# Kernel optimization log

Hardware: AMD Instinct MI355X
Metric: run time of the kernel (lower is better)

The kernel has to match this reference:

```python
import jax, jax.numpy as jnp
import numpy as np
import math

B, N, E, H, DEPTH, MLP_RATIO, A = 8, 1024, 768, 12, 6, 4, 7
F = MLP_RATIO * E


def _get_attention_slopes(n):
    def p2(n):
        start = 2 ** (-2 ** (-(math.log2(n) - 3)))
        return [start * start ** i for i in range(n)]
    if math.log2(n).is_integer():
        return p2(n)
    c = 2 ** math.floor(math.log2(n))
    return p2(c) + _get_attention_slopes(2 * c)[0::2][: n - c]


def _ln(x, scale, bias, eps=1e-6):
    m = jnp.mean(x, axis=-1, keepdims=True)
    v = jnp.var(x, axis=-1, keepdims=True)
    return (x - m) * jax.lax.rsqrt(v + eps) * scale + bias


def setup_inputs() -> dict:
    key = jax.random.key(0)
    ks = jax.random.split(key, 8)
    s = 0.02
    return {
        "x": jax.random.normal(ks[0], (B, N, E), jnp.float32),
        "ln1_scale": jnp.ones((DEPTH, E), jnp.float32),
        "ln1_bias": jnp.zeros((DEPTH, E), jnp.float32),
        "wqkv": jax.random.normal(ks[1], (DEPTH, E, 3 * E), jnp.float32) * s,
        "bqkv": jnp.zeros((DEPTH, 3 * E), jnp.float32),
        "wo": jax.random.normal(ks[2], (DEPTH, E, E), jnp.float32) * s,
        "bo": jnp.zeros((DEPTH, E), jnp.float32),
        "ln2_scale": jnp.ones((DEPTH, E), jnp.float32),
        "ln2_bias": jnp.zeros((DEPTH, E), jnp.float32),
        "w1": jax.random.normal(ks[3], (DEPTH, E, F), jnp.float32) * s,
        "w2": jax.random.normal(ks[4], (DEPTH, F, E), jnp.float32) * s,
        "lnf_scale": jnp.ones((E,), jnp.float32),
        "lnf_bias": jnp.zeros((E,), jnp.float32),
        "head_w1": jax.random.normal(ks[5], (E, E), jnp.float32) * s,
        "head_b1": jnp.zeros((E,), jnp.float32),
        "head_w2": jax.random.normal(ks[6], (E, A), jnp.float32) * s,
    }


def reference(x, ln1_scale, ln1_bias, wqkv, bqkv, wo, bo, ln2_scale, ln2_bias, w1, w2, lnf_scale, lnf_bias, head_w1, head_b1, head_w2):
    b, n, e = x.shape
    h = H
    dh = e // h
    scale = dh ** (-0.5)
    # ALiBi bias: slopes[h] * key-position (exactly as original code computes it)
    slopes = jnp.asarray(_get_attention_slopes(h), x.dtype)
    pos_bias = slopes[None, :, None, None] * jnp.arange(n, dtype=x.dtype)[None, None, None, :]
    causal = jnp.tril(jnp.ones((n, n), bool))[None, None]  # [1,1,n,n]
    big_neg = jnp.finfo(x.dtype).min

    depth = ln1_scale.shape[0]
    for i in range(depth):
        y = _ln(x, ln1_scale[i], ln1_bias[i])
        qkv = y @ wqkv[i] + bqkv[i]
        q, k, v = jnp.split(qkv, 3, axis=-1)
        q = q.reshape(b, n, h, dh).transpose(0, 2, 1, 3)  # b h n d
        k = k.reshape(b, n, h, dh).transpose(0, 2, 1, 3)
        v = v.reshape(b, n, h, dh).transpose(0, 2, 1, 3)
        att = jnp.einsum('bhnd,bhmd->bhnm', q, k) * scale + pos_bias
        att = jnp.where(causal, att, big_neg)
        att = jax.nn.softmax(att, axis=-1)
        o = jnp.einsum('bhnm,bhmd->bhnd', att, v)
        o = o.transpose(0, 2, 1, 3).reshape(b, n, e)
        x = x + (o @ wo[i] + bo[i])
        y = _ln(x, ln2_scale[i], ln2_bias[i])
        y = jax.nn.gelu(y @ w1[i])  # flax default: tanh-approx gelu; FF has no bias
        x = x + y @ w2[i]
    x = _ln(x, lnf_scale, lnf_bias)
    actions = jax.nn.relu(x @ head_w1 + head_b1) @ head_w2
    return actions
```

## Files before the change

kernel.cpp:

```cpp
#include <hip/hip_runtime.h>
#include <hip/hip_bf16.h>
#include <cstdint>

#define DEV __device__ __forceinline__

typedef __bf16 bf16x8 __attribute__((ext_vector_type(8)));
typedef float f32x4 __attribute__((ext_vector_type(4)));
typedef unsigned short u16;
typedef u16 u16x8 __attribute__((ext_vector_type(8)));
typedef u16 u16x4 __attribute__((ext_vector_type(4)));
typedef uint32_t u32x2 __attribute__((ext_vector_type(2)));

DEV u16 f2bf(float f) {
  union { float f; uint32_t u; } a; a.f = f;
  uint32_t u = a.u + 0x7fffu + ((a.u >> 16) & 1u);
  return (u16)(u >> 16);
}
DEV float b2f(u16 v) {
  union { uint32_t u; float f; } a; a.u = ((uint32_t)v) << 16;
  return a.f;
}

DEV float fexp2(float x) {
#if __has_builtin(__builtin_amdgcn_exp2f)
  return __builtin_amdgcn_exp2f(x);
#else
  return __expf(x * 0.69314718056f);
#endif
}

DEV uint32_t cvtpk(float lo, float hi) {
  uint32_t r;
  asm("v_cvt_pk_bf16_f32 %0, %1, %2" : "=v"(r) : "v"(lo), "v"(hi));
  return r;
}

DEV void gload16(const void* g, void* lds) {
  __builtin_amdgcn_global_load_lds((__attribute__((address_space(1))) void*)g,
                                   (__attribute__((address_space(3))) void*)lds,
                                   16, 0, 0);
}

DEV void nts8(u16* p, u16x8 v) {
  __builtin_nontemporal_store(v, (u16x8*)p);
}

struct TMat { const float* src; u16* dst; int K; int N; int t0; };
struct TArgs { TMat m[26]; int nmat; };

__global__ __launch_bounds__(256) void transpose_all(TArgs args) {
  __shared__ float tile[64][65];
  const int bid = blockIdx.x;
  int i = 0;
  #pragma unroll 1
  for (int t = 1; t < args.nmat; ++t) if (bid >= args.m[t].t0) i = t;
  const TMat mm = args.m[i];
  const int tid = bid - mm.t0;
  const int ntx = mm.N >> 6;
  const int tx = tid % ntx, ty = tid / ntx;
  const int n0 = tx * 64, k0 = ty * 64;
  const int c = threadIdx.x & 63, r0 = threadIdx.x >> 6;
  #pragma unroll
  for (int s = 0; s < 16; ++s) {
    int r = r0 + s * 4;
    tile[r][c] = mm.src[(size_t)(k0 + r) * mm.N + n0 + c];
  }
  __syncthreads();
  #pragma unroll
  for (int s = 0; s < 16; ++s) {
    int rr = r0 + s * 4;
    mm.dst[(size_t)(n0 + rr) * mm.K + k0 + c] = f2bf(tile[c][rr]);
  }
}

__global__ __launch_bounds__(256) void ln_kernel(const float* __restrict__ x,
                                                 const float* __restrict__ sc,
                                                 const float* __restrict__ bi,
                                                 u16* __restrict__ y, int Mtok) {
  const int bid = blockIdx.x;
  const int tok = ((bid & 7) << 10) + ((bid >> 3) << 2) + (threadIdx.x >> 6);
  const int l = threadIdx.x & 63;
  if (tok >= Mtok) return;
  const float4* row = (const float4*)(x + (size_t)tok * 768);
  float4 a = row[l], b = row[l + 64], cc = row[l + 128];
  float s = a.x + a.y + a.z + a.w + b.x + b.y + b.z + b.w + cc.x + cc.y + cc.z + cc.w;
  float q = a.x*a.x + a.y*a.y + a.z*a.z + a.w*a.w
          + b.x*b.x + b.y*b.y + b.z*b.z + b.w*b.w
          + cc.x*cc.x + cc.y*cc.y + cc.z*cc.z + cc.w*cc.w;
  #pragma unroll
  for (int off = 1; off < 64; off <<= 1) { s += __shfl_xor(s, off); q += __shfl_xor(q, off); }
  const float mean = s * (1.f / 768.f);
  const float var = q * (1.f / 768.f) - mean * mean;
  const float r = rsqrtf(var + 1e-6f);
  u16* yr = y + (size_t)tok * 768;
  #pragma unroll
  for (int p = 0; p < 3; ++p) {
    const int col0 = 4 * (l + 64 * p);
    float4 v = (p == 0) ? a : (p == 1) ? b : cc;
    float4 scv = *(const float4*)(sc + col0);
    float4 biv = *(const float4*)(bi + col0);
    u16x4 o;
    o[0] = f2bf((v.x - mean) * r * scv.x + biv.x);
    o[1] = f2bf((v.y - mean) * r * scv.y + biv.y);
    o[2] = f2bf((v.z - mean) * r * scv.z + biv.z);
    o[3] = f2bf((v.w - mean) * r * scv.w + biv.w);
    *(u16x4*)(yr + col0) = o;
  }
}

enum { EPI_BF16 = 0, EPI_RESID = 1, EPI_GELU = 2, EPI_RELU = 3 };

__global__ __launch_bounds__(256, 2) void gemm128(
    const u16* __restrict__ A, const u16* __restrict__ Bt,
    const float* __restrict__ bias, const float* __restrict__ resid,
    float* __restrict__ outF, u16* __restrict__ outB,
    int N, int K, int nxb, int epi) {
  __shared__ u16 smem[32768];
  const int tid = threadIdx.x;
  const int w = tid >> 6, l = tid & 63;

  const int nwg = gridDim.x;
  const int flat = blockIdx.x;
  const int wg = (flat & 7) * (nwg >> 3) + (flat >> 3);
  const int bx = wg % nxb, by = wg / nxb;
  const int m0 = by << 7, n0 = bx << 7;

  const int wr = (w >> 1) << 6, wc = (w & 1) << 6;
  const int cl = l & 15, g = l >> 4;
  f32x4 acc[4][4] = {};

  const int lrow = l >> 3;
  const int scol = ((l & 7) ^ lrow) << 3;
  const u16* agp = A  + (size_t)(m0 + (w << 5) + lrow) * K + scol;
  const u16* bgp = Bt + (size_t)(n0 + (w << 5) + lrow) * K + scol;
  const int ldso = w << 11;
  const int nkt = K >> 6;

  #pragma unroll
  for (int q = 0; q < 4; ++q) {
    gload16(agp + (size_t)(q * 8) * K, &smem[ldso + (q << 9)]);
    gload16(bgp + (size_t)(q * 8) * K, &smem[16384 + ldso + (q << 9)]);
  }

  const int sw = cl & 7;
  for (int kt = 0; kt < nkt; ++kt) {
    const int cur = kt & 1;
    if (kt + 1 < nkt) {
      const size_t koff = (size_t)(kt + 1) << 6;
      const int nb = (cur ^ 1) << 13;
      #pragma unroll
      for (int q = 0; q < 4; ++q) {
        gload16(agp + koff + (size_t)(q * 8) * K, &smem[nb + ldso + (q << 9)]);
        gload16(bgp + koff + (size_t)(q * 8) * K, &smem[16384 + nb + ldso + (q << 9)]);
      }
      asm volatile("s_waitcnt vmcnt(8)" ::: "memory");
    } else {
      asm volatile("s_waitcnt vmcnt(0)" ::: "memory");
    }
    __builtin_amdgcn_s_barrier();
    __builtin_amdgcn_sched_barrier(0);
    const u16* Ab = &smem[cur << 13];
    const u16* Bb = &smem[16384 + (cur << 13)];
    #pragma unroll
    for (int ks = 0; ks < 2; ++ks) {
      bf16x8 af[4], bfr[4];
      const int ps = (((ks << 2) | g) ^ sw) << 3;
      #pragma unroll
      for (int mt = 0; mt < 4; ++mt)
        af[mt] = *(const bf16x8*)(Ab + ((wr + mt * 16 + cl) << 6) + ps);
      #pragma unroll
      for (int nt = 0; nt < 4; ++nt)
        bfr[nt] = *(const bf16x8*)(Bb + ((wc + nt * 16 + cl) << 6) + ps);
      #pragma unroll
      for (int mt = 0; mt < 4; ++mt)
        #pragma unroll
        for (int nt = 0; nt < 4; ++nt)
          acc[mt][nt] = __builtin_amdgcn_mfma_f32_16x16x32_bf16(af[mt], bfr[nt], acc[mt][nt], 0, 0, 0);
    }
    asm volatile("s_waitcnt lgkmcnt(0)" ::: "memory");
    __builtin_amdgcn_s_barrier();
  }

  float* scr = (float*)smem + w * 1056;
  const int rg = g << 2;
  const int er = l >> 3;
  const int ec0 = (l & 7) << 3;
  #pragma unroll
  for (int mt = 0; mt < 4; ++mt) {
    #pragma unroll
    for (int nt = 0; nt < 4; ++nt)
      #pragma unroll
      for (int j = 0; j < 4; ++j)
        scr[(rg + j) * 66 + nt * 16 + cl] = acc[mt][nt][j];
    #pragma unroll
    for (int t = 0; t < 2; ++t) {
      const int r = (t << 3) + er;
      const int grow = m0 + wr + mt * 16 + r;
      const int gcol = n0 + wc + ec0;
      float v[8];
      #pragma unroll
      for (int u = 0; u < 8; ++u) v[u] = scr[r * 66 + ec0 + u];
      if (bias) {
        #pragma unroll
        for (int u = 0; u < 8; ++u) v[u] += bias[gcol + u];
      }
      if (epi == EPI_RESID) {
        const float* rp = resid + (size_t)grow * N + gcol;
        float* op = outF + (size_t)grow * N + gcol;
        float4 o0, o1;
        o0.x = v[0] + rp[0]; o0.y = v[1] + rp[1]; o0.z = v[2] + rp[2]; o0.w = v[3] + rp[3];
        o1.x = v[4] + rp[4]; o1.y = v[5] + rp[5]; o1.z = v[6] + rp[6]; o1.w = v[7] + rp[7];
        *(float4*)op = o0;
        *(float4*)(op + 4) = o1;
      } else {
        u16x8 ov;
        #pragma unroll
        for (int u = 0; u < 8; ++u) {
          float x = v[u];
          if (epi == EPI_GELU) {
            const float e = __expf(-(1.5957691216f * x + 0.0713548163f * x * x * x));
            x = x / (1.f + e);
          } else if (epi == EPI_RELU) {
            x = fmaxf(x, 0.f);
          }
          ov[u] = f2bf(x);
        }
        if (epi == EPI_BF16 || epi == EPI_GELU)
          nts8(outB + (size_t)grow * N + gcol, ov);
        else
          *(u16x8*)(outB + (size_t)grow * N + gcol) = ov;
      }
    }
  }
}

__global__ __launch_bounds__(512, 2) void attn_kernel(const u16* __restrict__ qkv,
                                                      u16* __restrict__ o) {
  __shared__ u16 Ksm[2][4096];
  __shared__ u16 Vt[2][64][68];
  __shared__ u16 P[8][16][72];
  const int flat = blockIdx.x;
  const int b = flat & 7;
  const int rr = flat >> 3;
  const int h = rr >> 3;
  const int j = rr & 7;
  const int tid = threadIdx.x;
  const int w = tid >> 6, l = tid & 63;
  const int cl = l & 15, lg = l >> 4;
  const int qtile = (w < 4) ? j : 15 - j;
  const int q0 = qtile * 64 + (w & 3) * 16;
  const int rowg = q0 + cl;
  const float log2e = 1.44269504f;
  const float scale2 = 0.125f * log2e;
  const float slope = (h < 8) ? exp2f(-(float)(h + 1)) : exp2f(-0.5f - (float)(h - 8));
  const float slope2 = slope * log2e;
  const size_t rs_ = 2304;
  const size_t bbase = (size_t)b * 1024 * rs_;

  const u16* qp = qkv + bbase + (size_t)rowg * rs_ + h * 64 + lg * 8;
  bf16x8 qa0 = *(const bf16x8*)qp;
  bf16x8 qa1 = *(const bf16x8*)(qp + 32);

  float m_r = -1e30f, l_r = 0.f;
  f32x4 oacc[4];
  #pragma unroll
  for (int d = 0; d < 4; ++d) oacc[d] = (f32x4){0.f, 0.f, 0.f, 0.f};

  const u16* ksrc = qkv + bbase + (size_t)(tid >> 3) * rs_ + 768 + h * 64 +
                    (((tid & 7) ^ ((tid >> 3) & 7)) << 3);
  const int vd0 = w << 3;
  const u16* vbase = qkv + bbase + (size_t)l * rs_ + 1536 + h * 64 + vd0;

  const int nkv = 16 - j;
  gload16(ksrc, &Ksm[0][w << 9]);
  u16x8 vreg = *(const u16x8*)vbase;
  __syncthreads();

  const int sw = cl & 7;
  const int ps0 = (lg ^ sw) << 3;
  const int ps1 = ps0 ^ 32;

  for (int kv = 0; kv < nkv; ++kv) {
    const int buf = kv & 1;
    #pragma unroll
    for (int i = 0; i < 8; ++i) Vt[buf][vd0 + i][l] = vreg[i];
    u16x8 vnext = vreg;
    if (kv + 1 < nkv) {
      gload16(ksrc + (size_t)(kv + 1) * 64 * rs_, &Ksm[buf ^ 1][w << 9]);
      vnext = *(const u16x8*)(vbase + (size_t)(kv + 1) * 64 * rs_);
    }

    const bool active = (kv <= qtile);
    bf16x8 pa0, pa1;
    if (active) {
      const u16* Kb = &Ksm[buf][0];
      f32x4 pp[4];
      float pm = -3.0e38f;
      __builtin_amdgcn_s_setprio(1);
      #pragma unroll
      for (int nt = 0; nt < 4; ++nt) {
        const int row = nt * 16 + cl;
        bf16x8 bk0 = *(const bf16x8*)(Kb + (row << 6) + ps0);
        bf16x8 bk1 = *(const bf16x8*)(Kb + (row << 6) + ps1);
        f32x4 s = (f32x4){0.f, 0.f, 0.f, 0.f};
        s = __builtin_amdgcn_mfma_f32_16x16x32_bf16(bk0, qa0, s, 0, 0, 0);
        s = __builtin_amdgcn_mfma_f32_16x16x32_bf16(bk1, qa1, s, 0, 0, 0);
        const int kb = kv * 64 + nt * 16 + (lg << 2);
        #pragma unroll
        for (int jj = 0; jj < 4; ++jj) {
          const int colg = kb + jj;
          float v = s[jj] * scale2 + slope2 * (float)colg;
          pp[nt][jj] = (colg <= rowg) ? v : -3.0e38f;
        }
        pm = fmaxf(pm, fmaxf(fmaxf(pp[nt][0], pp[nt][1]),
                             fmaxf(pp[nt][2], pp[nt][3])));
      }
      __builtin_amdgcn_s_setprio(0);
      pm = fmaxf(pm, __shfl_xor(pm, 16));
      pm = fmaxf(pm, __shfl_xor(pm, 32));
      const float mnew = fmaxf(m_r, pm);
      const float al = fexp2(m_r - mnew);
      m_r = mnew;
      float rs = 0.f;
      #pragma unroll
      for (int nt = 0; nt < 4; ++nt) {
        #pragma unroll
        for (int jj = 0; jj < 4; ++jj) {
          float p = fexp2(pp[nt][jj] - m_r);
          pp[nt][jj] = p;
          rs += p;
        }
      }
      rs += __shfl_xor(rs, 16);
      rs += __shfl_xor(rs, 32);
      l_r = l_r * al + rs;
      float a4[4];
      #pragma unroll
      for (int jj = 0; jj < 4; ++jj) a4[jj] = __shfl(al, (lg << 2) + jj);
      #pragma unroll
      for (int d = 0; d < 4; ++d)
        #pragma unroll
        for (int jj = 0; jj < 4; ++jj) oacc[d][jj] *= a4[jj];
      #pragma unroll
      for (int nt = 0; nt < 4; ++nt) {
        u32x2 pr;
        pr[0] = cvtpk(pp[nt][0], pp[nt][1]);
        pr[1] = cvtpk(pp[nt][2], pp[nt][3]);
        *(u32x2*)&P[w][cl][nt * 16 + (lg << 2)] = pr;
      }
      pa0 = *(const bf16x8*)&P[w][cl][lg * 8];
      pa1 = *(const bf16x8*)&P[w][cl][32 + lg * 8];
    }

    __syncthreads();

    if (active) {
      __builtin_amdgcn_s_setprio(1);
      #pragma unroll
      for (int d = 0; d < 4; ++d) {
        bf16x8 bv0 = *(const bf16x8*)&Vt[buf][d * 16 + cl][lg * 8];
        bf16x8 bv1 = *(const bf16x8*)&Vt[buf][d * 16 + cl][32 + lg * 8];
        oacc[d] = __builtin_amdgcn_mfma_f32_16x16x32_bf16(pa0, bv0, oacc[d], 0, 0, 0);
        oacc[d] = __builtin_amdgcn_mfma_f32_16x16x32_bf16(pa1, bv1, oacc[d], 0, 0, 0);
      }
      __builtin_amdgcn_s_setprio(0);
    }
    vreg = vnext;
  }

  const float linv = 1.f / l_r;
  float i4[4];
  #pragma unroll
  for (int jj = 0; jj < 4; ++jj) i4[jj] = __shfl(linv, (lg << 2) + jj);
  u16* op = o + ((size_t)b * 1024 + q0) * 768 + h * 64;
  #pragma unroll
  for (int d = 0; d < 4; ++d)
    #pragma unroll
    for (int jj = 0; jj < 4; ++jj)
      op[(size_t)((lg << 2) + jj) * 768 + d * 16 + cl] = f2bf(oacc[d][jj] * i4[jj]);
}

__global__ __launch_bounds__(256) void head2_kernel(const u16* __restrict__ act,
                                                    const float* __restrict__ w,
                                                    float* __restrict__ out, int Mtok) {
  const int bid = blockIdx.x;
  const int tok = ((bid & 7) << 10) + ((bid >> 3) << 2) + (threadIdx.x >> 6);
  const int l = threadIdx.x & 63;
  if (tok >= Mtok) return;
  float s[7] = {0.f, 0.f, 0.f, 0.f, 0.f, 0.f, 0.f};
  const u16* ar = act + (size_t)tok * 768;
  #pragma unroll
  for (int i = 0; i < 12; ++i) {
    const int k = l + i * 64;
    const float a = b2f(ar[k]);
    #pragma unroll
    for (int j = 0; j < 7; ++j) s[j] += a * w[k * 7 + j];
  }
  #pragma unroll
  for (int off = 32; off; off >>= 1)
    #pragma unroll
    for (int j = 0; j < 7; ++j) s[j] += __shfl_down(s[j], off);
  if (l == 0) {
    #pragma unroll
    for (int j = 0; j < 7; ++j) out[(size_t)tok * 7 + j] = s[j];
  }
}

extern "C" void kernel_launch(void* const* d_in, const int* in_sizes, int n_in,
                              void* d_out, int out_size, void* d_ws, size_t ws_size,
                              hipStream_t stream) {
  const float* x_in = (const float*)d_in[0];
  const float* ln1s = (const float*)d_in[1];
  const float* ln1b = (const float*)d_in[2];
  const float* wqkv = (const float*)d_in[3];
  const float* bqkv = (const float*)d_in[4];
  const float* wo   = (const float*)d_in[5];
  const float* bo   = (const float*)d_in[6];
  const float* ln2s = (const float*)d_in[7];
  const float* ln2b = (const float*)d_in[8];
  const float* w1   = (const float*)d_in[9];
  const float* w2   = (const float*)d_in[10];
  const float* lnfs = (const float*)d_in[11];
  const float* lnfb = (const float*)d_in[12];
  const float* hw1  = (const float*)d_in[13];
  const float* hb1  = (const float*)d_in[14];
  const float* hw2  = (const float*)d_in[15];
  float* out = (float*)d_out;

  const int Mtok = 8192, E = 768, E3 = 2304, F = 3072, DEPTH = 6;

  char* ws = (char*)d_ws;
  size_t off = 0;
  auto alloc = [&](size_t bytes) -> char* {
    char* p = ws + off; off += (bytes + 255) & ~(size_t)255; return p;
  };
  u16*  wqkvt = (u16*)alloc((size_t)DEPTH * E3 * E * 2);
  u16*  wot   = (u16*)alloc((size_t)DEPTH * E * E * 2);
  u16*  w1t   = (u16*)alloc((size_t)DEPTH * F * E * 2);
  u16*  w2t   = (u16*)alloc((size_t)DEPTH * E * F * 2);
  u16*  hw1t  = (u16*)alloc((size_t)E * E * 2);
  float* xb   = (float*)alloc((size_t)Mtok * E * 4);
  u16*  yb    = (u16*)alloc((size_t)Mtok * E * 2);
  u16*  big   = (u16*)alloc((size_t)Mtok * F * 2);
  (void)ws_size; (void)in_sizes; (void)n_in; (void)out_size;

  TArgs ta; int nm = 0; int t0 = 0;
  auto add = [&](const float* s, u16* d, int K, int N) {
    ta.m[nm].src = s; ta.m[nm].dst = d; ta.m[nm].K = K; ta.m[nm].N = N; ta.m[nm].t0 = t0;
    t0 += (N / 64) * (K / 64); ++nm;
  };
  for (int i = 0; i < DEPTH; ++i) add(wqkv + (size_t)i * E * E3, wqkvt + (size_t)i * E3 * E, E, E3);
  for (int i = 0; i < DEPTH; ++i) add(wo + (size_t)i * E * E, wot + (size_t)i * E * E, E, E);
  for (int i = 0; i < DEPTH; ++i) add(w1 + (size_t)i * E * F, w1t + (size_t)i * F * E, E, F);
  for (int i = 0; i < DEPTH; ++i) add(w2 + (size_t)i * F * E, w2t + (size_t)i * E * F, F, E);
  add(hw1, hw1t, E, E);
  ta.nmat = nm;
  transpose_all<<<t0, 256, 0, stream>>>(ta);

  u16* qkvb = big;
  for (int i = 0; i < DEPTH; ++i) {
    const float* xsrc = (i == 0) ? x_in : xb;
    ln_kernel<<<Mtok / 4, 256, 0, stream>>>(xsrc, ln1s + i * E, ln1b + i * E, yb, Mtok);
    gemm128<<<18 * 64, 256, 0, stream>>>(yb, wqkvt + (size_t)i * E3 * E, bqkv + (size_t)i * E3,
                                         nullptr, nullptr, qkvb, E3, E, 18, EPI_BF16);
    attn_kernel<<<768, 512, 0, stream>>>(qkvb, yb);
    gemm128<<<6 * 64, 256, 0, stream>>>(yb, wot + (size_t)i * E * E, bo + (size_t)i * E,
                                        xsrc, xb, nullptr, E, E, 6, EPI_RESID);
    ln_kernel<<<Mtok / 4, 256, 0, stream>>>(xb, ln2s + i * E, ln2b + i * E, yb, Mtok);
    gemm128<<<24 * 64, 256, 0, stream>>>(yb, w1t + (size_t)i * F * E, nullptr,
                                         nullptr, nullptr, big, F, E, 24, EPI_GELU);
    gemm128<<<6 * 64, 256, 0, stream>>>(big, w2t + (size_t)i * E * F, nullptr,
                                        xb, xb, nullptr, E, F, 6, EPI_RESID);
  }
  ln_kernel<<<Mtok / 4, 256, 0, stream>>>(xb, lnfs, lnfb, yb, Mtok);
  gemm128<<<6 * 64, 256, 0, stream>>>(yb, hw1t, hb1, nullptr, nullptr, big,
                                      E, E, 6, EPI_RELU);
  head2_kernel<<<Mtok / 4, 256, 0, stream>>>(big, hw2, out, Mtok);
}
```

Measured before the change: 1.477 ms.

## Store residual stream in bf16 and skip unneeded softmax rescales

The residual stream buffer changes from fp32 to bf16. The input is converted once, LayerNorm reads bf16, and the residual GEMM epilogues read and write bf16, which halves residual memory traffic. The bf16 packing now uses the hardware cvt_pk instruction. In attention, the running-max rescale of the accumulators is skipped when no new row max exceeds the old one by a threshold, saving exp and multiply work. Accumulating the residual in bf16 over 12 layers loses precision and could hurt accuracy.

```diff
diff --git a/kernel.cpp b/kernel.cpp
--- a/kernel.cpp
+++ b/kernel.cpp
@@ -10,6 +10,7 @@
 typedef u16 u16x8 __attribute__((ext_vector_type(8)));
 typedef u16 u16x4 __attribute__((ext_vector_type(4)));
 typedef uint32_t u32x2 __attribute__((ext_vector_type(2)));
+typedef uint32_t u32x4 __attribute__((ext_vector_type(4)));
 
 DEV u16 f2bf(float f) {
   union { float f; uint32_t u; } a; a.f = f;
@@ -39,10 +40,6 @@
   __builtin_amdgcn_global_load_lds((__attribute__((address_space(1))) void*)g,
                                    (__attribute__((address_space(3))) void*)lds,
                                    16, 0, 0);
-}
-
-DEV void nts8(u16* p, u16x8 v) {
-  __builtin_nontemporal_store(v, (u16x8*)p);
 }
 
 struct TMat { const float* src; u16* dst; int K; int N; int t0; };
@@ -73,7 +70,18 @@
   }
 }
 
-__global__ __launch_bounds__(256) void ln_kernel(const float* __restrict__ x,
+__global__ __launch_bounds__(256) void f2b_kernel(const float4* __restrict__ in,
+                                                  u32x4* __restrict__ out, int n8) {
+  const int i = blockIdx.x * 256 + threadIdx.x;
+  if (i >= n8) return;
+  float4 a = in[2 * i], b = in[2 * i + 1];
+  u32x4 o;
+  o[0] = cvtpk(a.x, a.y); o[1] = cvtpk(a.z, a.w);
+  o[2] = cvtpk(b.x, b.y); o[3] = cvtpk(b.z, b.w);
+  out[i] = o;
+}
+
+__global__ __launch_bounds__(256) void ln_kernel(const u16* __restrict__ x,
                                                  const float* __restrict__ sc,
                                                  const float* __restrict__ bi,
                                                  u16* __restrict__ y, int Mtok) {
@@ -81,40 +89,50 @@
   const int tok = ((bid & 7) << 10) + ((bid >> 3) << 2) + (threadIdx.x >> 6);
   const int l = threadIdx.x & 63;
   if (tok >= Mtok) return;
-  const float4* row = (const float4*)(x + (size_t)tok * 768);
-  float4 a = row[l], b = row[l + 64], cc = row[l + 128];
-  float s = a.x + a.y + a.z + a.w + b.x + b.y + b.z + b.w + cc.x + cc.y + cc.z + cc.w;
-  float q = a.x*a.x + a.y*a.y + a.z*a.z + a.w*a.w
-          + b.x*b.x + b.y*b.y + b.z*b.z + b.w*b.w
-          + cc.x*cc.x + cc.y*cc.y + cc.z*cc.z + cc.w*cc.w;
+  const u16* row = x + (size_t)tok * 768;
+  u16x8 v0 = *(const u16x8*)(row + l * 8);
+  u16x4 v1 = *(const u16x4*)(row + 512 + l * 4);
+  float f[12];
+  #pragma unroll
+  for (int i = 0; i < 8; ++i) f[i] = b2f(v0[i]);
+  #pragma unroll
+  for (int i = 0; i < 4; ++i) f[8 + i] = b2f(v1[i]);
+  float s = 0.f, q = 0.f;
+  #pragma unroll
+  for (int i = 0; i < 12; ++i) { s += f[i]; q += f[i] * f[i]; }
   #pragma unroll
   for (int off = 1; off < 64; off <<= 1) { s += __shfl_xor(s, off); q += __shfl_xor(q, off); }
   const float mean = s * (1.f / 768.f);
   const float var = q * (1.f / 768.f) - mean * mean;
   const float r = rsqrtf(var + 1e-6f);
+  float4 s0 = *(const float4*)(sc + l * 8);
+  float4 s1 = *(const float4*)(sc + l * 8 + 4);
+  float4 s2 = *(const float4*)(sc + 512 + l * 4);
+  float4 b0 = *(const float4*)(bi + l * 8);
+  float4 b1 = *(const float4*)(bi + l * 8 + 4);
+  float4 b2 = *(const float4*)(bi + 512 + l * 4);
+  float g[12];
+  g[0] = (f[0]-mean)*r*s0.x + b0.x;  g[1] = (f[1]-mean)*r*s0.y + b0.y;
+  g[2] = (f[2]-mean)*r*s0.z + b0.z;  g[3] = (f[3]-mean)*r*s0.w + b0.w;
+  g[4] = (f[4]-mean)*r*s1.x + b1.x;  g[5] = (f[5]-mean)*r*s1.y + b1.y;
+  g[6] = (f[6]-mean)*r*s1.z + b1.z;  g[7] = (f[7]-mean)*r*s1.w + b1.w;
+  g[8] = (f[8]-mean)*r*s2.x + b2.x;  g[9] = (f[9]-mean)*r*s2.y + b2.y;
+  g[10] = (f[10]-mean)*r*s2.z + b2.z; g[11] = (f[11]-mean)*r*s2.w + b2.w;
   u16* yr = y + (size_t)tok * 768;
-  #pragma unroll
-  for (int p = 0; p < 3; ++p) {
-    const int col0 = 4 * (l + 64 * p);
-    float4 v = (p == 0) ? a : (p == 1) ? b : cc;
-    float4 scv = *(const float4*)(sc + col0);
-    float4 biv = *(const float4*)(bi + col0);
-    u16x4 o;
-    o[0] = f2bf((v.x - mean) * r * scv.x + biv.x);
-    o[1] = f2bf((v.y - mean) * r * scv.y + biv.y);
-    o[2] = f2bf((v.z - mean) * r * scv.z + biv.z);
-    o[3] = f2bf((v.w - mean) * r * scv.w + biv.w);
-    *(u16x4*)(yr + col0) = o;
-  }
+  u32x4 o;
+  o[0] = cvtpk(g[0], g[1]); o[1] = cvtpk(g[2], g[3]);
+  o[2] = cvtpk(g[4], g[5]); o[3] = cvtpk(g[6], g[7]);
+  *(u32x4*)(yr + l * 8) = o;
+  u32x2 o2; o2[0] = cvtpk(g[8], g[9]); o2[1] = cvtpk(g[10], g[11]);
+  *(u32x2*)(yr + 512 + l * 4) = o2;
 }
 
 enum { EPI_BF16 = 0, EPI_RESID = 1, EPI_GELU = 2, EPI_RELU = 3 };
 
 __global__ __launch_bounds__(256, 2) void gemm128(
     const u16* __restrict__ A, const u16* __restrict__ Bt,
-    const float* __restrict__ bias, const float* __restrict__ resid,
-    float* __restrict__ outF, u16* __restrict__ outB,
-    int N, int K, int nxb, int epi) {
+    const float* __restrict__ bias, const u16* __restrict__ residB,
+    u16* __restrict__ outB, int N, int K, int nxb, int epi) {
   __shared__ u16 smem[32768];
   const int tid = threadIdx.x;
   const int w = tid >> 6, l = tid & 63;
@@ -205,31 +223,28 @@
         for (int u = 0; u < 8; ++u) v[u] += bias[gcol + u];
       }
       if (epi == EPI_RESID) {
-        const float* rp = resid + (size_t)grow * N + gcol;
-        float* op = outF + (size_t)grow * N + gcol;
-        float4 o0, o1;
-        o0.x = v[0] + rp[0]; o0.y = v[1] + rp[1]; o0.z = v[2] + rp[2]; o0.w = v[3] + rp[3];
-        o1.x = v[4] + rp[4]; o1.y = v[5] + rp[5]; o1.z = v[6] + rp[6]; o1.w = v[7] + rp[7];
-        *(float4*)op = o0;
-        *(float4*)(op + 4) = o1;
-      } else {
-        u16x8 ov;
+        u16x8 rv = *(const u16x8*)(residB + (size_t)grow * N + gcol);
+        #pragma unroll
+        for (int u = 0; u < 8; ++u) v[u] += b2f(rv[u]);
+      } else if (epi == EPI_GELU) {
         #pragma unroll
         for (int u = 0; u < 8; ++u) {
-          float x = v[u];
-          if (epi == EPI_GELU) {
-            const float e = __expf(-(1.5957691216f * x + 0.0713548163f * x * x * x));
-            x = x / (1.f + e);
-          } else if (epi == EPI_RELU) {
-            x = fmaxf(x, 0.f);
-          }
-          ov[u] = f2bf(x);
+          const float x = v[u];
+          const float e = __expf(-(1.5957691216f * x + 0.0713548163f * x * x * x));
+          v[u] = x / (1.f + e);
         }
-        if (epi == EPI_BF16 || epi == EPI_GELU)
-          nts8(outB + (size_t)grow * N + gcol, ov);
-        else
-          *(u16x8*)(outB + (size_t)grow * N + gcol) = ov;
-      }
+      } else if (epi == EPI_RELU) {
+        #pragma unroll
+        for (int u = 0; u < 8; ++u) v[u] = fmaxf(v[u], 0.f);
+      }
+      u32x4 ov;
+      ov[0] = cvtpk(v[0], v[1]); ov[1] = cvtpk(v[2], v[3]);
+      ov[2] = cvtpk(v[4], v[5]); ov[3] = cvtpk(v[6], v[7]);
+      u32x4* op = (u32x4*)(outB + (size_t)grow * N + gcol);
+      if (epi == EPI_BF16 || epi == EPI_GELU)
+        __builtin_nontemporal_store(ov, op);
+      else
+        *op = ov;
     }
   }
 }
@@ -318,9 +333,19 @@
       __builtin_amdgcn_s_setprio(0);
       pm = fmaxf(pm, __shfl_xor(pm, 16));
       pm = fmaxf(pm, __shfl_xor(pm, 32));
-      const float mnew = fmaxf(m_r, pm);
-      const float al = fexp2(m_r - mnew);
-      m_r = mnew;
+      if (!__all(pm <= m_r + 11.54f)) {
+        const float mnew = fmaxf(m_r, pm);
+        const float al = fexp2(m_r - mnew);
+        m_r = mnew;
+        l_r *= al;
+        float a4[4];
+        #pragma unroll
+        for (int jj = 0; jj < 4; ++jj) a4[jj] = __shfl(al, (lg << 2) + jj);
+        #pragma unroll
+        for (int d = 0; d < 4; ++d)
+          #pragma unroll
+          for (int jj = 0; jj < 4; ++jj) oacc[d][jj] *= a4[jj];
+      }
       float rs = 0.f;
       #pragma unroll
       for (int nt = 0; nt < 4; ++nt) {
@@ -333,14 +358,7 @@
       }
       rs += __shfl_xor(rs, 16);
       rs += __shfl_xor(rs, 32);
-      l_r = l_r * al + rs;
-      float a4[4];
-      #pragma unroll
-      for (int jj = 0; jj < 4; ++jj) a4[jj] = __shfl(al, (lg << 2) + jj);
-      #pragma unroll
-      for (int d = 0; d < 4; ++d)
-        #pragma unroll
-        for (int jj = 0; jj < 4; ++jj) oacc[d][jj] *= a4[jj];
+      l_r += rs;
       #pragma unroll
       for (int nt = 0; nt < 4; ++nt) {
         u32x2 pr;
@@ -439,7 +457,7 @@
   u16*  w1t   = (u16*)alloc((size_t)DEPTH * F * E * 2);
   u16*  w2t   = (u16*)alloc((size_t)DEPTH * E * F * 2);
   u16*  hw1t  = (u16*)alloc((size_t)E * E * 2);
-  float* xb   = (float*)alloc((size_t)Mtok * E * 4);
+  u16*  xb    = (u16*)alloc((size_t)Mtok * E * 2);
   u16*  yb    = (u16*)alloc((size_t)Mtok * E * 2);
   u16*  big   = (u16*)alloc((size_t)Mtok * F * 2);
   (void)ws_size; (void)in_sizes; (void)n_in; (void)out_size;
@@ -457,23 +475,25 @@
   ta.nmat = nm;
   transpose_all<<<t0, 256, 0, stream>>>(ta);
 
+  f2b_kernel<<<(Mtok * E / 8 + 255) / 256, 256, 0, stream>>>(
+      (const float4*)x_in, (u32x4*)xb, Mtok * E / 8);
+
   u16* qkvb = big;
   for (int i = 0; i < DEPTH; ++i) {
-    const float* xsrc = (i == 0) ? x_in : xb;
-    ln_kernel<<<Mtok / 4, 256, 0, stream>>>(xsrc, ln1s + i * E, ln1b + i * E, yb, Mtok);
+    ln_kernel<<<Mtok / 4, 256, 0, stream>>>(xb, ln1s + i * E, ln1b + i * E, yb, Mtok);
     gemm128<<<18 * 64, 256, 0, stream>>>(yb, wqkvt + (size_t)i * E3 * E, bqkv + (size_t)i * E3,
-                                         nullptr, nullptr, qkvb, E3, E, 18, EPI_BF16);
+                                         nullptr, qkvb, E3, E, 18, EPI_BF16);
     attn_kernel<<<768, 512, 0, stream>>>(qkvb, yb);
     gemm128<<<6 * 64, 256, 0, stream>>>(yb, wot + (size_t)i * E * E, bo + (size_t)i * E,
-                                        xsrc, xb, nullptr, E, E, 6, EPI_RESID);
+                                        xb, xb, E, E, 6, EPI_RESID);
     ln_kernel<<<Mtok / 4, 256, 0, stream>>>(xb, ln2s + i * E, ln2b + i * E, yb, Mtok);
     gemm128<<<24 * 64, 256, 0, stream>>>(yb, w1t + (size_t)i * F * E, nullptr,
-                                         nullptr, nullptr, big, F, E, 24, EPI_GELU);
+                                         nullptr, big, F, E, 24, EPI_GELU);
     gemm128<<<6 * 64, 256, 0, stream>>>(big, w2t + (size_t)i * E * F, nullptr,
-                                        xb, xb, nullptr, E, F, 6, EPI_RESID);
+                                        xb, xb, E, F, 6, EPI_RESID);
   }
   ln_kernel<<<Mtok / 4, 256, 0, stream>>>(xb, lnfs, lnfb, yb, Mtok);
-  gemm128<<<6 * 64, 256, 0, stream>>>(yb, hw1t, hb1, nullptr, nullptr, big,
+  gemm128<<<6 * 64, 256, 0, stream>>>(yb, hw1t, hb1, nullptr, big,
                                       E, E, 6, EPI_RELU);
   head2_kernel<<<Mtok / 4, 256, 0, stream>>>(big, hw2, out, Mtok);
 }
```

Result: faster. 1.410 ms (-4.5%).
